# Kernel optimization log

Hardware: AMD Instinct MI355X
Metric: run time of the kernel (lower is better)

Reference implementation:

```python
import jax, jax.numpy as jnp
import numpy as np


def _rope_tables(T, half):
    # theta_i = 10000^(-i/half), standard RoPE frequencies for head_size=2*half
    thetas = 10000.0 ** (-jnp.arange(half, dtype=jnp.float32) / half)  # (half,)
    ang = jnp.arange(T, dtype=jnp.float32)[:, None] * thetas[None, :]  # (T, half)
    return jnp.sin(ang), jnp.cos(ang)


def _apply_rope(x, sin, cos):
    # x: (B, H, T, hs); sin/cos: (T, hs//2). Interleaved pair rotation.
    xe = x[..., 0::2]
    xo = x[..., 1::2]
    s = sin[None, None, :, :]
    c = cos[None, None, :, :]
    re = xe * c - xo * s
    ro = xe * s + xo * c
    return jnp.stack([re, ro], axis=-1).reshape(x.shape)


def setup_inputs() -> dict:
    key = jax.random.key(0)
    ks = jax.random.split(key, 5)
    B, T, C, H = 4, 2048, 1024, 16
    scale = 1.0 / np.sqrt(C)
    x = jax.random.normal(ks[0], (B, T, C), dtype=jnp.float32)
    Wqkv = jax.random.normal(ks[1], (C, 3 * C), dtype=jnp.float32) * scale
    bqkv = jax.random.normal(ks[2], (3 * C,), dtype=jnp.float32) * 0.01
    Wout = jax.random.normal(ks[3], (C, C), dtype=jnp.float32) * scale
    bout = jax.random.normal(ks[4], (C,), dtype=jnp.float32) * 0.01
    return {"x": x, "Wqkv": Wqkv, "bqkv": bqkv, "Wout": Wout, "bout": bout,
            "num_heads": H}


def reference(x, Wqkv, bqkv, Wout, bout, num_heads) -> jnp.ndarray:
    B, T, C = x.shape
    H = num_heads
    hs = C // H
    norm = 1.0 / np.sqrt(hs)

    qkv = x @ Wqkv + bqkv                       # (B, T, 3C)
    qkv = qkv.reshape(B, T, 3, H, hs)
    qkv = jnp.transpose(qkv, (0, 3, 2, 1, 4))   # (B, H, 3, T, hs) = transpose(1,3)
    q, k, v = qkv[:, :, 0], qkv[:, :, 1], qkv[:, :, 2]  # each (B, H, T, hs)

    sin, cos = _rope_tables(T, hs // 2)
    q = _apply_rope(q, sin, cos)
    k = _apply_rope(k, sin, cos)

    att = jnp.einsum('bhqd,bhkd->bhqk', q, k) * norm  # (B, H, T, T)
    causal = jnp.triu(jnp.ones((T, T), dtype=bool), k=1)
    att = jnp.where(causal[None, None], -jnp.inf, att)
    att_prob = jax.nn.softmax(att, axis=-1)

    out = jnp.einsum('bhqk,bhkd->bhqd', att_prob, v)  # (B, H, T, hs)
    out = jnp.transpose(out, (0, 2, 1, 3)).reshape(B, T, C)
    return out @ Wout + bout
```

## Files before the change

kernel.cpp:

```cpp
#include <hip/hip_runtime.h>
#include <math.h>

#define B_   4
#define T_   2048
#define C_   1024
#define H_   16
#define HS   64
#define HALF 32
#define QKV_N (3 * C_)
#define M_    (B_ * T_)

using bf16x8 = __attribute__((ext_vector_type(8))) short;
using f32x4  = __attribute__((ext_vector_type(4))) float;
using f32x16 = __attribute__((ext_vector_type(16))) float;
using u16x4  = __attribute__((ext_vector_type(4))) unsigned short;
using u32x2  = __attribute__((ext_vector_type(2))) unsigned int;

__device__ __forceinline__ unsigned short f2bf(float f) {
    unsigned u = __builtin_bit_cast(unsigned, f);
    u = (u + 0x7FFFu + ((u >> 16) & 1u)) >> 16;
    return (unsigned short)u;
}
__device__ __forceinline__ float bf2f(unsigned short b) {
    return __builtin_bit_cast(float, (unsigned)b << 16);
}
__device__ __forceinline__ unsigned cvtpk_bf16(float lo, float hi_) {
    unsigned r;
    asm("v_cvt_pk_bf16_f32 %0, %1, %2" : "=v"(r) : "v"(lo), "v"(hi_));
    return r;
}
__device__ __forceinline__ void gload16(const void* g, void* l) {
    __builtin_amdgcn_global_load_lds(
        (const __attribute__((address_space(1))) unsigned int*)g,
        (__attribute__((address_space(3))) unsigned int*)l, 16, 0, 0);
}
#define WAIT_VMCNT_8() asm volatile("s_waitcnt vmcnt(8)" ::: "memory")
#define WAIT_VMCNT_4() asm volatile("s_waitcnt vmcnt(4)" ::: "memory")
#define WAIT_VMCNT_0() asm volatile("s_waitcnt vmcnt(0)" ::: "memory")
#define WAIT_LGKM_0()  asm volatile("s_waitcnt lgkmcnt(0)" ::: "memory")

#if __has_builtin(__builtin_amdgcn_exp2f)
#define EXP2(x) __builtin_amdgcn_exp2f(x)
#else
#define EXP2(x) exp2f(x)
#endif
#define FMAX3(a, b, c) fmaxf(fmaxf((a), (b)), (c))

#define QSCALE 0.18033688011112042f

__global__ __launch_bounds__(256) void prep2_kernel(
    const float* __restrict__ x, unsigned short* __restrict__ xb,
    float2* __restrict__ tab,
    const float* __restrict__ Wqkv, const float* __restrict__ Wout,
    unsigned short* __restrict__ Wqkvt, unsigned short* __restrict__ Woutt)
{
    __shared__ float tile[32][33];
    const int bid = blockIdx.x;
    if (bid < 4096) {
        const size_t i = ((size_t)bid * 256 + threadIdx.x) * 8;
        const float4 a = *reinterpret_cast<const float4*>(&x[i]);
        const float4 b = *reinterpret_cast<const float4*>(&x[i + 4]);
        bf16x8 v;
        v[0] = f2bf(a.x); v[1] = f2bf(a.y); v[2] = f2bf(a.z); v[3] = f2bf(a.w);
        v[4] = f2bf(b.x); v[5] = f2bf(b.y); v[6] = f2bf(b.z); v[7] = f2bf(b.w);
        *reinterpret_cast<bf16x8*>(&xb[i]) = v;
        return;
    }
    if (bid < 4352) {
        const int idx = (bid - 4096) * 256 + threadIdx.x;
        const int t = idx / HALF;
        const int i = idx % HALF;
        const float theta = powf(10000.0f, -(float)i / (float)HALF);
        const float ang = (float)t * theta;
        float sn, cs;
        sincosf(ang, &sn, &cs);
        tab[idx] = make_float2(sn, cs);
        return;
    }
    const float* W;
    unsigned short* Wt;
    int N, k0, n0;
    if (bid < 7424) {
        const int r0 = bid - 4352;
        W = Wqkv; Wt = Wqkvt; N = QKV_N;
        n0 = (r0 % 96) * 32; k0 = (r0 / 96) * 32;
    } else {
        const int r0 = bid - 7424;
        W = Wout; Wt = Woutt; N = C_;
        n0 = (r0 % 32) * 32; k0 = (r0 / 32) * 32;
    }
    const int K = C_;
    const int r = threadIdx.x / 32;
    const int c = threadIdx.x % 32;
    #pragma unroll
    for (int it = 0; it < 4; ++it)
        tile[r + it * 8][c] = W[(size_t)(k0 + r + it * 8) * N + n0 + c];
    __syncthreads();
    #pragma unroll
    for (int it = 0; it < 4; ++it)
        Wt[(size_t)(n0 + r + it * 8) * K + k0 + c] = f2bf(tile[c][r + it * 8]);
}

template <int N, int K, bool BF16OUT, bool ROPE, bool VSPLIT>
__global__ __launch_bounds__(512, 1) void gemm_8ph_kernel(
    const unsigned short* __restrict__ A, const unsigned short* __restrict__ Bt,
    const float* __restrict__ bias, const float2* __restrict__ tab,
    void* __restrict__ Cout, unsigned short* __restrict__ vt, int nbx, int nby)
{
    __shared__ unsigned short As0[2][128 * 64];
    __shared__ unsigned short As1[2][128 * 64];
    __shared__ unsigned short Bs0[2][128 * 64];
    __shared__ unsigned short Bs1[2][128 * 64];

    const int tid  = threadIdx.x;
    const int lane = tid & 63;
    const int wave = tid >> 6;
    const int wr   = wave >> 2;
    const int wc   = wave & 3;
    const int l15  = lane & 15;
    const int l4   = lane >> 4;

    const int bid  = blockIdx.x;
    const int xcd  = bid & 7;
    const int w    = bid >> 3;
    const int cpr  = nbx >> 1;
    const int rpr  = nby >> 2;
    const int by   = ((xcd >> 1) * rpr) + (w / cpr);
    const int bx   = ((xcd & 1) * cpr) + (w % cpr);
    const int row0 = by * 256;
    const int col0 = bx * 256;

    const int lr0 = tid >> 3,          sl0 = tid & 7;
    const int lr1 = (tid + 512) >> 3,  sl1 = (tid + 512) & 7;
    const int kc0 = (sl0 ^ (lr0 & 7)) * 8;
    const int kc1 = (sl1 ^ (lr1 & 7)) * 8;
    const int dA0 = tid * 8;
    const int dA1 = (tid + 512) * 8;
    const unsigned short* apS0 = &A[(size_t)(row0 + (lr0 >> 6) * 128 + (lr0 & 63)) * K + kc0];
    const unsigned short* apS1 = &A[(size_t)(row0 + (lr1 >> 6) * 128 + (lr1 & 63)) * K + kc1];
    const unsigned short* bpS0 = &Bt[(size_t)(col0 + (lr0 >> 5) * 64 + (lr0 & 31)) * K + kc0];
    const unsigned short* bpS1 = &Bt[(size_t)(col0 + (lr1 >> 5) * 64 + (lr1 & 31)) * K + kc1];

    auto stA0 = [&](int buf, int t) {
        gload16(apS0 + t * 64,            &As0[buf][dA0]);
        gload16(apS1 + t * 64,            &As0[buf][dA1]);
    };
    auto stA1 = [&](int buf, int t) {
        gload16(apS0 + t * 64 + 64 * K,   &As1[buf][dA0]);
        gload16(apS1 + t * 64 + 64 * K,   &As1[buf][dA1]);
    };
    auto stB0 = [&](int buf, int t) {
        gload16(bpS0 + t * 64,            &Bs0[buf][dA0]);
        gload16(bpS1 + t * 64,            &Bs0[buf][dA1]);
    };
    auto stB1 = [&](int buf, int t) {
        gload16(bpS0 + t * 64 + 32 * K,   &Bs1[buf][dA0]);
        gload16(bpS1 + t * 64 + 32 * K,   &Bs1[buf][dA1]);
    };

    int aoff[2][4], boff[2][2];
    #pragma unroll
    for (int kk = 0; kk < 2; ++kk) {
        #pragma unroll
        for (int mi = 0; mi < 4; ++mi) {
            const int lr = wr * 64 + mi * 16 + l15;
            aoff[kk][mi] = lr * 64 + (((kk * 4 + l4) ^ (lr & 7)) * 8);
        }
        #pragma unroll
        for (int nj = 0; nj < 2; ++nj) {
            const int lr = wc * 32 + nj * 16 + l15;
            boff[kk][nj] = lr * 64 + (((kk * 4 + l4) ^ (lr & 7)) * 8);
        }
    }

    f32x4 acc[8][4] = {};
    constexpr int nt = K / 64;

    stA0(0, 0); stB0(0, 0); stB1(0, 0); stA1(0, 0);
    WAIT_VMCNT_4();
    __builtin_amdgcn_s_barrier();

    bf16x8 a[2][4], b01[2][2], b23[2][2];

    for (int t = 0; t < nt; ++t) {
        const int cur = t & 1;
        const int nxt = cur ^ 1;
        const int tn  = (t + 1 < nt) ? t + 1 : 0;

        #pragma unroll
        for (int kk = 0; kk < 2; ++kk) {
            #pragma unroll
            for (int mi = 0; mi < 4; ++mi)
                a[kk][mi] = *reinterpret_cast<const bf16x8*>(&As0[cur][aoff[kk][mi]]);
            #pragma unroll
            for (int nj = 0; nj < 2; ++nj)
                b01[kk][nj] = *reinterpret_cast<const bf16x8*>(&Bs0[cur][boff[kk][nj]]);
        }
        stA0(nxt, tn);
        WAIT_VMCNT_4();
        __builtin_amdgcn_s_barrier();
        WAIT_LGKM_0();
        __builtin_amdgcn_sched_barrier(0);
        __builtin_amdgcn_s_setprio(1);
        #pragma unroll
        for (int kk = 0; kk < 2; ++kk)
            #pragma unroll
            for (int mi = 0; mi < 4; ++mi)
                #pragma unroll
                for (int nj = 0; nj < 2; ++nj)
                    acc[mi][nj] = __builtin_amdgcn_mfma_f32_16x16x32_bf16(
                        a[kk][mi], b01[kk][nj], acc[mi][nj], 0, 0, 0);
        __builtin_amdgcn_s_setprio(0);
        __builtin_amdgcn_sched_barrier(0);
        __builtin_amdgcn_s_barrier();

        #pragma unroll
        for (int kk = 0; kk < 2; ++kk)
            #pragma unroll
            for (int nj = 0; nj < 2; ++nj)
                b23[kk][nj] = *reinterpret_cast<const bf16x8*>(&Bs1[cur][boff[kk][nj]]);
        stB0(nxt, tn);
        WAIT_VMCNT_4();
        __builtin_amdgcn_s_barrier();
        WAIT_LGKM_0();
        __builtin_amdgcn_sched_barrier(0);
        __builtin_amdgcn_s_setprio(1);
        #pragma unroll
        for (int kk = 0; kk < 2; ++kk)
            #pragma unroll
            for (int mi = 0; mi < 4; ++mi)
                #pragma unroll
                for (int nj = 0; nj < 2; ++nj)
                    acc[mi][2 + nj] = __builtin_amdgcn_mfma_f32_16x16x32_bf16(
                        a[kk][mi], b23[kk][nj], acc[mi][2 + nj], 0, 0, 0);
        __builtin_amdgcn_s_setprio(0);
        __builtin_amdgcn_sched_barrier(0);
        __builtin_amdgcn_s_barrier();

        #pragma unroll
        for (int kk = 0; kk < 2; ++kk)
            #pragma unroll
            for (int mi = 0; mi < 4; ++mi)
                a[kk][mi] = *reinterpret_cast<const bf16x8*>(&As1[cur][aoff[kk][mi]]);
        stB1(nxt, tn);
        WAIT_VMCNT_4();
        __builtin_amdgcn_s_barrier();
        WAIT_LGKM_0();
        __builtin_amdgcn_sched_barrier(0);
        __builtin_amdgcn_s_setprio(1);
        #pragma unroll
        for (int kk = 0; kk < 2; ++kk)
            #pragma unroll
            for (int mi = 0; mi < 4; ++mi)
                #pragma unroll
                for (int nj = 0; nj < 2; ++nj)
                    acc[4 + mi][nj] = __builtin_amdgcn_mfma_f32_16x16x32_bf16(
                        a[kk][mi], b01[kk][nj], acc[4 + mi][nj], 0, 0, 0);
        __builtin_amdgcn_s_setprio(0);
        __builtin_amdgcn_sched_barrier(0);
        __builtin_amdgcn_s_barrier();

        stA1(nxt, tn);
        WAIT_VMCNT_4();
        __builtin_amdgcn_s_barrier();
        __builtin_amdgcn_sched_barrier(0);
        __builtin_amdgcn_s_setprio(1);
        #pragma unroll
        for (int kk = 0; kk < 2; ++kk)
            #pragma unroll
            for (int mi = 0; mi < 4; ++mi)
                #pragma unroll
                for (int nj = 0; nj < 2; ++nj)
                    acc[4 + mi][2 + nj] = __builtin_amdgcn_mfma_f32_16x16x32_bf16(
                        a[kk][mi], b23[kk][nj], acc[4 + mi][2 + nj], 0, 0, 0);
        __builtin_amdgcn_s_setprio(0);
        __builtin_amdgcn_sched_barrier(0);
        __builtin_amdgcn_s_barrier();
    }
    WAIT_VMCNT_0();

    float bv[4];
    #pragma unroll
    for (int nf = 0; nf < 4; ++nf)
        bv[nf] = bias[col0 + wc * 64 + nf * 16 + l15];

    if (VSPLIT && col0 >= 2 * C_) {
        #pragma unroll
        for (int mf = 0; mf < 8; ++mf) {
            const int rowb = row0 + wr * 128 + mf * 16 + l4 * 4;
            const int b  = rowb >> 11;
            const int t0 = rowb & (T_ - 1);
            #pragma unroll
            for (int nf = 0; nf < 4; ++nf) {
                const int cv = col0 - 2 * C_ + wc * 64 + nf * 16 + l15;
                u16x4 pack;
                #pragma unroll
                for (int r = 0; r < 4; ++r)
                    pack[r] = f2bf(acc[mf][nf][r] + bv[nf]);
                *reinterpret_cast<u16x4*>(
                    &vt[((size_t)(b * H_ * HS + cv)) * T_ + t0]) = pack;
            }
        }
        return;
    }

    const bool doRope = ROPE && (col0 < 2 * C_);
    const bool doScaleQ = ROPE && (col0 < C_);

    #pragma unroll
    for (int mf = 0; mf < 8; ++mf) {
        #pragma unroll
        for (int r = 0; r < 4; ++r) {
            const int row = row0 + wr * 128 + mf * 16 + l4 * 4 + r;
            const int t   = row & (T_ - 1);
            #pragma unroll
            for (int nf = 0; nf < 4; ++nf) {
                const int col = col0 + wc * 64 + nf * 16 + l15;
                float v = acc[mf][nf][r] + bv[nf];
                if (doRope) {
                    const float partner = __shfl_xor(v, 1);
                    const float2 sc = tab[t * HALF + ((col & 63) >> 1)];
                    v = v * sc.y + ((col & 1) ? partner : -partner) * sc.x;
                }
                if (doScaleQ) v *= QSCALE;
                if (BF16OUT)
                    ((unsigned short*)Cout)[(size_t)row * N + col] = f2bf(v);
                else
                    ((float*)Cout)[(size_t)row * N + col] = v;
            }
        }
    }
}

__global__ __launch_bounds__(256, 2) void attn_mfma5_kernel(
    const unsigned short* __restrict__ qkv,
    const unsigned short* __restrict__ vt,
    unsigned short* __restrict__ out)
{
    __shared__ unsigned short Ks[2][128 * 64];
    __shared__ unsigned short Vs[2][64 * 128];

    const int idx = blockIdx.x;
    const int bh  = idx & 63;
    const int qp  = idx >> 6;
    const int b   = bh >> 4;
    const int h   = bh & 15;
    const int qtA = qp;
    const int qtB = 15 - qp;

    const int tid  = threadIdx.x;
    const int lane = tid & 63;
    const int w    = tid >> 6;
    const int l31  = lane & 31;
    const int hi   = lane >> 5;

    const int qwA = qtA * 128 + w * 32;
    const int qgA = qwA + l31;
    const int qwB = qtB * 128 + w * 32;
    const int qgB = qwB + l31;

    bf16x8 aqA[4], aqB[4];
    {
        const unsigned short* qpA = &qkv[(size_t)(b * T_ + qgA) * QKV_N + h * HS + hi * 8];
        const unsigned short* qpB = &qkv[(size_t)(b * T_ + qgB) * QKV_N + h * HS + hi * 8];
        #pragma unroll
        for (int kc = 0; kc < 4; ++kc) {
            aqA[kc] = *reinterpret_cast<const bf16x8*>(qpA + kc * 16);
            aqB[kc] = *reinterpret_cast<const bf16x8*>(qpB + kc * 16);
        }
    }

    f32x16 accA0 = {}, accA1 = {}, accB0 = {}, accB1 = {};
    float mA = -INFINITY, lA = 0.f, mB = -INFINITY, lB = 0.f;

    auto stageKV = [&](int buf, int it) {
        #pragma unroll
        for (int n = 0; n < 4; ++n) {
            const int r  = n * 32 + (tid >> 3);
            const int sk = ((tid & 7) ^ (r & 7)) * 8;
            gload16(&qkv[(size_t)(b * T_ + it * 128 + r) * QKV_N + C_ + h * HS + sk],
                    &Ks[buf][(n * 256 + tid) * 8]);
        }
        #pragma unroll
        for (int n = 0; n < 4; ++n) {
            const int d  = n * 16 + (tid >> 4);
            const int sv = ((tid & 15) ^ (d & 7)) * 8;
            gload16(&vt[((size_t)(bh * HS + d)) * T_ + it * 128 + sv],
                    &Vs[buf][(n * 256 + tid) * 8]);
        }
    };

    auto process = [&](const unsigned short* Kb, const unsigned short* Vb,
                       const bf16x8* aq, f32x16& a0, f32x16& a1,
                       float& mval, float& lval, int qw, int qg, int kbase) {
        f32x16 s[4] = {};
        __builtin_amdgcn_s_setprio(1);
        #pragma unroll
        for (int kc = 0; kc < 4; ++kc) {
            const int bo = kc * 32 + hi * 16;
            #pragma unroll
            for (int g = 0; g < 4; ++g) {
                const int rj = g * 32 + l31;
                const bf16x8 ak = *reinterpret_cast<const bf16x8*>(
                    &Kb[rj * 64 + ((bo ^ ((rj & 7) << 4)) >> 1)]);
                s[g] = __builtin_amdgcn_mfma_f32_32x32x16_bf16(ak, aq[kc], s[g], 0, 0, 0);
            }
        }
        __builtin_amdgcn_s_setprio(0);

        if (kbase + 127 > qw) {
            #pragma unroll
            for (int g = 0; g < 4; ++g) {
                #pragma unroll
                for (int r = 0; r < 16; ++r) {
                    const int j0 = kbase + g * 32 + (r & 3) + 8 * (r >> 2) + 4 * hi;
                    if (j0 > qg) s[g][r] = -INFINITY;
                }
            }
        }

        float tg[4];
        #pragma unroll
        for (int g = 0; g < 4; ++g) {
            const float v0 = FMAX3(s[g][0],  s[g][1],  s[g][2]);
            const float v1 = FMAX3(s[g][3],  s[g][4],  s[g][5]);
            const float v2 = FMAX3(s[g][6],  s[g][7],  s[g][8]);
            const float v3 = FMAX3(s[g][9],  s[g][10], s[g][11]);
            const float v4 = FMAX3(s[g][12], s[g][13], s[g][14]);
            tg[g] = fmaxf(FMAX3(v0, v1, v2), FMAX3(v3, v4, s[g][15]));
        }
        float tm = fmaxf(fmaxf(tg[0], tg[1]), fmaxf(tg[2], tg[3]));
        tm = fmaxf(tm, __shfl_xor(tm, 32));

        const bool upd = (tm > mval + 8.f);
        if (__ballot(upd)) {
            const float nm = upd ? tm : mval;
            const float sf = EXP2(mval - nm);
            lval *= sf;
            #pragma unroll
            for (int r = 0; r < 16; ++r) { a0[r] *= sf; a1[r] *= sf; }
            mval = nm;
        }

        float rs0 = 0.f, rs1 = 0.f, rs2 = 0.f, rs3 = 0.f;
        #pragma unroll
        for (int r = 0; r < 16; ++r) {
            s[0][r] = EXP2(s[0][r] - mval); rs0 += s[0][r];
            s[1][r] = EXP2(s[1][r] - mval); rs1 += s[1][r];
            s[2][r] = EXP2(s[2][r] - mval); rs2 += s[2][r];
            s[3][r] = EXP2(s[3][r] - mval); rs3 += s[3][r];
        }
        float rs = (rs0 + rs1) + (rs2 + rs3);
        rs += __shfl_xor(rs, 32);
        lval += rs;

        #pragma unroll
        for (int g2 = 0; g2 < 2; ++g2) {
            #pragma unroll
            for (int jt = 0; jt < 2; ++jt) {
                const int g = g2 * 2 + jt;
                #pragma unroll
                for (int c = 0; c < 2; ++c) {
                    const int e = c * 8;
                    const unsigned pa = cvtpk_bf16(s[g][e + 0], s[g][e + 1]);
                    const unsigned pb = cvtpk_bf16(s[g][e + 2], s[g][e + 3]);
                    const unsigned pc = cvtpk_bf16(s[g][e + 4], s[g][e + 5]);
                    const unsigned pd = cvtpk_bf16(s[g][e + 6], s[g][e + 7]);
                    int4 bw;
#if __has_builtin(__builtin_amdgcn_permlane32_swap)
                    const u32x2 rx = __builtin_amdgcn_permlane32_swap(pa, pc, false, false);
                    const u32x2 ry = __builtin_amdgcn_permlane32_swap(pb, pd, false, false);
                    bw.x = (int)rx[0]; bw.y = (int)ry[0];
                    bw.z = (int)rx[1]; bw.w = (int)ry[1];
#else
                    const unsigned pas = (unsigned)__shfl_xor((int)pa, 32);
                    const unsigned pbs = (unsigned)__shfl_xor((int)pb, 32);
                    const unsigned pcs = (unsigned)__shfl_xor((int)pc, 32);
                    const unsigned pds = (unsigned)__shfl_xor((int)pd, 32);
                    bw.x = (int)(hi ? pcs : pa);
                    bw.y = (int)(hi ? pds : pb);
                    bw.z = (int)(hi ? pc  : pas);
                    bw.w = (int)(hi ? pd  : pbs);
#endif
                    const bf16x8 bfrag = __builtin_bit_cast(bf16x8, bw);

                    const int lslot = g2 * 8 + (jt * 2 + c) * 2 + hi;
                    const int d0 = l31;
                    const bf16x8 av0 = *reinterpret_cast<const bf16x8*>(
                        &Vb[d0 * 128 + (lslot ^ (d0 & 7)) * 8]);
                    const int d1 = 32 + l31;
                    const bf16x8 av1 = *reinterpret_cast<const bf16x8*>(
                        &Vb[d1 * 128 + (lslot ^ (d1 & 7)) * 8]);
                    __builtin_amdgcn_s_setprio(1);
                    a0 = __builtin_amdgcn_mfma_f32_32x32x16_bf16(av0, bfrag, a0, 0, 0, 0);
                    a1 = __builtin_amdgcn_mfma_f32_32x32x16_bf16(av1, bfrag, a1, 0, 0, 0);
                    __builtin_amdgcn_s_setprio(0);
                }
            }
        }
    };

    const int nIter = qtB + 1;
    stageKV(0, 0);
    for (int it = 0; it < nIter; ++it) {
        const int cur = it & 1;
        __builtin_amdgcn_sched_barrier(0);
        if (it + 1 < nIter) {
            stageKV(cur ^ 1, it + 1);
            WAIT_VMCNT_8();
        } else {
            WAIT_VMCNT_0();
        }
        __builtin_amdgcn_s_barrier();
        __builtin_amdgcn_sched_barrier(0);

        const unsigned short* Kb = &Ks[cur][0];
        const unsigned short* Vb = &Vs[cur][0];
        const int kbase = it * 128;
        if (kbase <= qwA + 31)
            process(Kb, Vb, aqA, accA0, accA1, mA, lA, qwA, qgA, kbase);
        if (kbase <= qwB + 31)
            process(Kb, Vb, aqB, accB0, accB1, mB, lB, qwB, qgB, kbase);
        __builtin_amdgcn_sched_barrier(0);
        __builtin_amdgcn_s_barrier();
    }

    {
        const float inv = 1.0f / lA;
        unsigned short* orow = &out[(size_t)(b * T_ + qgA) * C_ + h * HS];
        #pragma unroll
        for (int g = 0; g < 4; ++g) {
            uint2 wv;
            wv.x = cvtpk_bf16(accA0[4 * g + 0] * inv, accA0[4 * g + 1] * inv);
            wv.y = cvtpk_bf16(accA0[4 * g + 2] * inv, accA0[4 * g + 3] * inv);
            *reinterpret_cast<uint2*>(&orow[8 * g + 4 * hi]) = wv;
            uint2 wv1;
            wv1.x = cvtpk_bf16(accA1[4 * g + 0] * inv, accA1[4 * g + 1] * inv);
            wv1.y = cvtpk_bf16(accA1[4 * g + 2] * inv, accA1[4 * g + 3] * inv);
            *reinterpret_cast<uint2*>(&orow[32 + 8 * g + 4 * hi]) = wv1;
        }
    }
    {
        const float inv = 1.0f / lB;
        unsigned short* orow = &out[(size_t)(b * T_ + qgB) * C_ + h * HS];
        #pragma unroll
        for (int g = 0; g < 4; ++g) {
            uint2 wv;
            wv.x = cvtpk_bf16(accB0[4 * g + 0] * inv, accB0[4 * g + 1] * inv);
            wv.y = cvtpk_bf16(accB0[4 * g + 2] * inv, accB0[4 * g + 3] * inv);
            *reinterpret_cast<uint2*>(&orow[8 * g + 4 * hi]) = wv;
            uint2 wv1;
            wv1.x = cvtpk_bf16(accB1[4 * g + 0] * inv, accB1[4 * g + 1] * inv);
            wv1.y = cvtpk_bf16(accB1[4 * g + 2] * inv, accB1[4 * g + 3] * inv);
            *reinterpret_cast<uint2*>(&orow[32 + 8 * g + 4 * hi]) = wv1;
        }
    }
}

extern "C" void kernel_launch(void* const* d_in, const int* in_sizes, int n_in,
                              void* d_out, int out_size, void* d_ws, size_t ws_size,
                              hipStream_t stream)
{
    const float* x    = (const float*)d_in[0];
    const float* Wqkv = (const float*)d_in[1];
    const float* bqkv = (const float*)d_in[2];
    const float* Wout = (const float*)d_in[3];
    const float* bout = (const float*)d_in[4];
    float* out = (float*)d_out;

    char* ws = (char*)d_ws;
    unsigned short* qkvb  = (unsigned short*)ws;
    unsigned short* xb    = (unsigned short*)(ws + 50331648);
    unsigned short* attnb = (unsigned short*)(ws + 67108864);
    unsigned short* vt_g  = (unsigned short*)(ws + 83886080);
    unsigned short* Wqkvt = (unsigned short*)(ws + 100663296);
    unsigned short* Woutt = (unsigned short*)(ws + 106954752);
    float2* tab           = (float2*)(ws + 109051904);

    prep2_kernel<<<8448, 256, 0, stream>>>(x, xb, tab, Wqkv, Wout, Wqkvt, Woutt);

    gemm_8ph_kernel<QKV_N, C_, true, true, true>
        <<<(M_ / 256) * (QKV_N / 256), 512, 0, stream>>>(
        xb, Wqkvt, bqkv, tab, qkvb, vt_g, QKV_N / 256, M_ / 256);

    attn_mfma5_kernel<<<B_ * H_ * (T_ / 256), 256, 0, stream>>>(qkvb, vt_g, attnb);

    gemm_8ph_kernel<C_, C_, false, false, false>
        <<<(M_ / 256) * (C_ / 256), 512, 0, stream>>>(
        attnb, Woutt, bout, nullptr, out, nullptr, C_ / 256, M_ / 256);
}
```

Baseline: 172.4 us.

## Use smaller 128x128 tile GEMM for output projection to improve CU occupancy

Adds a lighter double-buffered 128x128-tile MFMA GEMM kernel with 256 threads and XCD-aware block mapping, and uses it for the output projection instead of the 256x256 eight-phase kernel. The old launch produced only 128 blocks, fewer than the GPU's compute units. The new tiling launches 512 blocks with up to 4 blocks per CU. The trade-off is lower per-block data reuse and more global/LDS traffic per FLOP.

```diff
diff --git a/kernel.cpp b/kernel.cpp
--- a/kernel.cpp
+++ b/kernel.cpp
@@ -323,6 +323,116 @@
                     v = v * sc.y + ((col & 1) ? partner : -partner) * sc.x;
                 }
                 if (doScaleQ) v *= QSCALE;
+                if (BF16OUT)
+                    ((unsigned short*)Cout)[(size_t)row * N + col] = f2bf(v);
+                else
+                    ((float*)Cout)[(size_t)row * N + col] = v;
+            }
+        }
+    }
+}
+
+template <int N, int K, bool BF16OUT>
+__global__ __launch_bounds__(256, 4) void gemm_2ph_kernel(
+    const unsigned short* __restrict__ A, const unsigned short* __restrict__ Bt,
+    const float* __restrict__ bias, void* __restrict__ Cout, int nbx, int nby)
+{
+    __shared__ unsigned short As[2][128 * 32];
+    __shared__ unsigned short Bs[2][128 * 32];
+
+    const int tid  = threadIdx.x;
+    const int lane = tid & 63;
+    const int wave = tid >> 6;
+    const int wr   = wave >> 1;
+    const int wc   = wave & 1;
+    const int l15  = lane & 15;
+    const int l4   = lane >> 4;
+
+    const int bid  = blockIdx.x;
+    const int xcd  = bid & 7;
+    const int w    = bid >> 3;
+    const int cpr  = nbx >> 1;
+    const int rpr  = nby >> 2;
+    const int by   = ((xcd >> 1) * rpr) + (w / cpr);
+    const int bx   = ((xcd & 1) * cpr) + (w % cpr);
+    const int row0 = by * 128;
+    const int col0 = bx * 128;
+
+    f32x4 acc[4][4] = {};
+
+    const int ar  = tid >> 2;
+    const int sl  = tid & 3;
+    const int swz = (sl ^ ((ar >> 1) & 3)) * 8;
+    const unsigned short* ap = &A[(size_t)(row0 + ar) * K + swz];
+    const unsigned short* bp = &Bt[(size_t)(col0 + ar) * K + swz];
+
+    auto stage = [&](int buf, int t) {
+        const unsigned short* a0 = ap + t * 32;
+        const unsigned short* b0 = bp + t * 32;
+        gload16(a0,          &As[buf][tid * 8]);
+        gload16(a0 + 64 * K, &As[buf][(tid + 256) * 8]);
+        gload16(b0,          &Bs[buf][tid * 8]);
+        gload16(b0 + 64 * K, &Bs[buf][(tid + 256) * 8]);
+    };
+
+    int aoff[4], boff[4];
+    #pragma unroll
+    for (int mi = 0; mi < 4; ++mi) {
+        const int lr = wr * 64 + mi * 16 + l15;
+        aoff[mi] = lr * 32 + ((l4 ^ ((lr >> 1) & 3)) * 8);
+    }
+    #pragma unroll
+    for (int nj = 0; nj < 4; ++nj) {
+        const int lr = wc * 64 + nj * 16 + l15;
+        boff[nj] = lr * 32 + ((l4 ^ ((lr >> 1) & 3)) * 8);
+    }
+
+    constexpr int nt = K / 32;
+    stage(0, 0);
+
+    for (int t = 0; t < nt; ++t) {
+        const int cur = t & 1;
+        if (t + 1 < nt) {
+            stage(cur ^ 1, t + 1);
+            WAIT_VMCNT_4();
+        } else {
+            WAIT_VMCNT_0();
+        }
+        __builtin_amdgcn_s_barrier();
+        __builtin_amdgcn_sched_barrier(0);
+
+        bf16x8 a[4], b[4];
+        #pragma unroll
+        for (int mi = 0; mi < 4; ++mi)
+            a[mi] = *reinterpret_cast<const bf16x8*>(&As[cur][aoff[mi]]);
+        #pragma unroll
+        for (int nj = 0; nj < 4; ++nj)
+            b[nj] = *reinterpret_cast<const bf16x8*>(&Bs[cur][boff[nj]]);
+        #pragma unroll
+        for (int mi = 0; mi < 4; ++mi)
+            #pragma unroll
+            for (int nj = 0; nj < 4; ++nj)
+                acc[mi][nj] = __builtin_amdgcn_mfma_f32_16x16x32_bf16(
+                    a[mi], b[nj], acc[mi][nj], 0, 0, 0);
+
+        __builtin_amdgcn_sched_barrier(0);
+        __builtin_amdgcn_s_barrier();
+    }
+
+    float bv[4];
+    #pragma unroll
+    for (int nj = 0; nj < 4; ++nj)
+        bv[nj] = bias[col0 + wc * 64 + nj * 16 + l15];
+
+    #pragma unroll
+    for (int mi = 0; mi < 4; ++mi) {
+        #pragma unroll
+        for (int r = 0; r < 4; ++r) {
+            const int row = row0 + wr * 64 + mi * 16 + l4 * 4 + r;
+            #pragma unroll
+            for (int nj = 0; nj < 4; ++nj) {
+                const int col = col0 + wc * 64 + nj * 16 + l15;
+                const float v = acc[mi][nj][r] + bv[nj];
                 if (BF16OUT)
                     ((unsigned short*)Cout)[(size_t)row * N + col] = f2bf(v);
                 else
@@ -585,7 +695,7 @@
 
     attn_mfma5_kernel<<<B_ * H_ * (T_ / 256), 256, 0, stream>>>(qkvb, vt_g, attnb);
 
-    gemm_8ph_kernel<C_, C_, false, false, false>
-        <<<(M_ / 256) * (C_ / 256), 512, 0, stream>>>(
-        attnb, Woutt, bout, nullptr, out, nullptr, C_ / 256, M_ / 256);
-}
+    gemm_2ph_kernel<C_, C_, false>
+        <<<(M_ / 128) * (C_ / 128), 256, 0, stream>>>(
+        attnb, Woutt, bout, out, C_ / 128, M_ / 128);
+}
```

Measured after the change: 166.9 us, median of 4. 3.2% less time.
